# Kernel optimization log

Measured on AMD Instinct MI355X. Metric: run time of the kernel, lower is better.

## Reference

```python
import jax, jax.numpy as jnp
import numpy as np

EPS = 1.1920929e-7  # torch.finfo(float32).eps, default for F.rms_norm
ATTN_SCALE = 0.1
ROPE_BASE = 10000.0


def _rms_norm(x):
    # F.rms_norm over last dim, no learned weight
    return x * jax.lax.rsqrt(jnp.mean(x * x, axis=-1, keepdims=True) + EPS)


def _rotary(x):
    # x: [B, T, H, D]; rotates halves as in the Rotary module
    T, D = x.shape[1], x.shape[3]
    half = D // 2
    inv_freq = 1.0 / (ROPE_BASE ** (jnp.arange(0, D, 2, dtype=jnp.float32) / D))  # [half]
    freqs = jnp.arange(T, dtype=jnp.float32)[:, None] * inv_freq[None, :]          # [T, half]
    cos = jnp.cos(freqs)[None, :, None, :]
    sin = jnp.sin(freqs)[None, :, None, :]
    x1, x2 = x[..., :half], x[..., half:]
    return jnp.concatenate([x1 * cos + x2 * sin, -x1 * sin + x2 * cos], axis=-1)


def setup_inputs() -> dict:
    key = jax.random.key(0)
    ks = jax.random.split(key, 8)
    B, T, dim, H, hd = 2, 2048, 1024, 16, 64
    gate_in = 12
    s = 1.0 / np.sqrt(dim)
    return {
        "x": jax.random.normal(ks[0], (B, T, dim), dtype=jnp.float32),
        "v1": jax.random.normal(ks[1], (B, T, H, hd), dtype=jnp.float32),
        "Wq": jax.random.uniform(ks[2], (dim, dim), jnp.float32, -s, s),
        "Wk": jax.random.uniform(ks[3], (dim, dim), jnp.float32, -s, s),
        "Wv": jax.random.uniform(ks[4], (dim, dim), jnp.float32, -s, s),
        "Wproj": jax.random.uniform(ks[5], (dim, dim), jnp.float32, -s, s),
        "Wg": jax.random.uniform(ks[6], (H, gate_in), jnp.float32,
                                  -1.0 / np.sqrt(gate_in), 1.0 / np.sqrt(gate_in)),
        "lamb": jnp.float32(0.5),
    }


def reference(x, v1, Wq, Wk, Wv, Wproj, Wg, lamb):
    B, T, dim = x.shape
    H, hd = v1.shape[2], v1.shape[3]
    q = (x @ Wq.T).reshape(B, T, H, hd)
    k = (x @ Wk.T).reshape(B, T, H, hd)
    v = (x @ Wv.T).reshape(B, T, H, hd)
    # value-residual mixing
    v = (1.0 - lamb) * v + lamb * v1
    # QK RMSNorm + RoPE
    q = _rotary(_rms_norm(q))
    k = _rotary(_rms_norm(k))
    # causal SDPA with fixed scale
    scores = jnp.einsum('bqhd,bkhd->bhqk', q, k) * ATTN_SCALE
    causal = jnp.tril(jnp.ones((T, T), dtype=bool))
    scores = jnp.where(causal[None, None], scores, jnp.float32(-jnp.inf))
    probs = jax.nn.softmax(scores, axis=-1)
    y = jnp.einsum('bhqk,bkhd->bqhd', probs, v)  # [B, T, H, hd]
    # sigmoid gate from first 12 channels of x
    gate = jax.nn.sigmoid(x[..., :Wg.shape[1]] @ Wg.T)  # [B, T, H]
    y = y * gate[..., None]
    y = y.reshape(B, T, H * hd) @ Wproj.T
    return y
```

## Files before the change

kernel.cpp:

```cpp
#include <hip/hip_runtime.h>
#include <math.h>


#define B_    2
#define T_    2048
#define DIM_  1024
#define H_    16
#define HD_   64
#define NROW  (B_ * T_)
#define EPS_  1.1920929e-07f
#define SCALE_ 0.1f
#define LOG2_10K 13.287712379549449f
#define INV2PI 0.15915494309189535f

typedef unsigned short u16;
typedef unsigned int   u32;
typedef __bf16 bf16x8 __attribute__((ext_vector_type(8)));
typedef __bf16 bf16x2 __attribute__((ext_vector_type(2)));
typedef float  f32x4  __attribute__((ext_vector_type(4)));

__device__ __forceinline__ u16 f2b(float f) {
  u32 u = __float_as_uint(f);
  u += 0x7fffu + ((u >> 16) & 1u);
  return (u16)(u >> 16);
}
__device__ __forceinline__ u32 pk2(float a, float b) {
#if __has_builtin(__builtin_amdgcn_cvt_pk_bf16_f32)
  bf16x2 r = __builtin_amdgcn_cvt_pk_bf16_f32(a, b);
  return __builtin_bit_cast(u32, r);
#else
  return (u32)f2b(a) | ((u32)f2b(b) << 16);
#endif
}
__device__ __forceinline__ void fast_sincos_rev(float rev, float* s, float* c) {
  const float r = rev - floorf(rev);
#if __has_builtin(__builtin_amdgcn_sinf) && __has_builtin(__builtin_amdgcn_cosf)
  *s = __builtin_amdgcn_sinf(r);
  *c = __builtin_amdgcn_cosf(r);
#else
  *s = __sinf(r * 6.283185307179586f);
  *c = __cosf(r * 6.283185307179586f);
#endif
}
#define MFMA16(a,b,c) __builtin_amdgcn_mfma_f32_16x16x32_bf16((a),(b),(c),0,0,0)

__global__ __launch_bounds__(256) void convert_all(
    const float* __restrict__ x, const float* __restrict__ Wq,
    const float* __restrict__ Wk, const float* __restrict__ Wv,
    const float* __restrict__ Wp,
    u16* __restrict__ xb, u16* __restrict__ wb ) {
  const int i = blockIdx.x * 256 + threadIdx.x;
  const float* src;
  u16* dst;
  int off;
  if (i < 1048576)       { src = x;  dst = xb;            off = i; }
  else if (i < 1310720)  { src = Wq; dst = wb;            off = i - 1048576; }
  else if (i < 1572864)  { src = Wk; dst = wb + 1048576;  off = i - 1310720; }
  else if (i < 1835008)  { src = Wv; dst = wb + 2097152;  off = i - 1572864; }
  else                   { src = Wp; dst = wb + 3145728;  off = i - 1835008; }
  const float4 f = ((const float4*)src)[off];
  uint2 o;
  o.x = pk2(f.x, f.y);
  o.y = pk2(f.z, f.w);
  ((uint2*)dst)[off] = o;
}

template <bool IS_PROJ>
__global__ __launch_bounds__(256) void gemm_rp(
    const u16* __restrict__ Ab, const u16* __restrict__ Wb,
    u16* __restrict__ qo, u16* __restrict__ ko, u16* __restrict__ vto,
    float* __restrict__ fo, const float* __restrict__ v1,
    const float* __restrict__ lambp) {
  __shared__ __attribute__((aligned(16))) unsigned char Asm[8192];
  __shared__ __attribute__((aligned(16))) unsigned char Bsm[8192];
  const int tid  = threadIdx.x;
  const int w    = tid >> 6;
  const int lane = tid & 63;
  const int lo = lane & 15, hi = lane >> 4;
  const int m0 = blockIdx.x << 7;
  const int by = blockIdx.y;
  const int mode = IS_PROJ ? 3 : (by >> 3);
  const int n0 = IS_PROJ ? (by << 7) : ((by & 7) << 7);
  const u16* W = IS_PROJ ? Wb : (Wb + (size_t)mode * (DIM_ * DIM_));

  const int wm = w & 1, wn = w >> 1;

  const u16* agA0 = Ab + (size_t)(m0 + (2 * w + 0) * 16 + lo) * DIM_ + (hi << 3);
  const u16* agA1 = Ab + (size_t)(m0 + (2 * w + 1) * 16 + lo) * DIM_ + (hi << 3);
  const u16* agB0 = W  + (size_t)(n0 + (2 * w + 0) * 16 + lo) * DIM_ + (hi << 3);
  const u16* agB1 = W  + (size_t)(n0 + (2 * w + 1) * 16 + lo) * DIM_ + (hi << 3);
  unsigned char* dA0 = Asm + (2 * w + 0) * 1024 + (lane << 4);
  unsigned char* dA1 = Asm + (2 * w + 1) * 1024 + (lane << 4);
  unsigned char* dB0 = Bsm + (2 * w + 0) * 1024 + (lane << 4);
  unsigned char* dB1 = Bsm + (2 * w + 1) * 1024 + (lane << 4);

  f32x4 acc[4][4];
#pragma unroll
  for (int i = 0; i < 4; ++i)
#pragma unroll
    for (int j = 0; j < 4; ++j) acc[i][j] = (f32x4){0.f, 0.f, 0.f, 0.f};

  uint4 ra0 = *(const uint4*)agA0;
  uint4 ra1 = *(const uint4*)agA1;
  uint4 rb0 = *(const uint4*)agB0;
  uint4 rb1 = *(const uint4*)agB1;
  agA0 += 32; agA1 += 32; agB0 += 32; agB1 += 32;

  for (int kc = 0; kc < DIM_; kc += 32) {
    __syncthreads();
    *(uint4*)dA0 = ra0;
    *(uint4*)dA1 = ra1;
    *(uint4*)dB0 = rb0;
    *(uint4*)dB1 = rb1;
    __syncthreads();
    if (kc + 32 < DIM_) {
      ra0 = *(const uint4*)agA0;
      ra1 = *(const uint4*)agA1;
      rb0 = *(const uint4*)agB0;
      rb1 = *(const uint4*)agB1;
      agA0 += 32; agA1 += 32; agB0 += 32; agB1 += 32;
    }
    bf16x8 bfr[4];
#pragma unroll
    for (int nt = 0; nt < 4; ++nt)
      bfr[nt] = *(const bf16x8*)(Bsm + (((wn * 4 + nt) * 64 + lane) << 4));
#pragma unroll
    for (int mt = 0; mt < 4; ++mt) {
      const bf16x8 af = *(const bf16x8*)(Asm + (((wm * 4 + mt) * 64 + lane) << 4));
#pragma unroll
      for (int nt = 0; nt < 4; ++nt)
        acc[mt][nt] = MFMA16(af, bfr[nt], acc[mt][nt]);
    }
  }

  const int head = (n0 >> 6) + wn;
  if (mode <= 1) {
    u16* C = (mode == 0) ? qo : ko;
    const float if0 = exp2f(-(float)lo * (LOG2_10K / 32.f)) * INV2PI;
    const float if1 = exp2f(-(float)(lo + 16) * (LOG2_10K / 32.f)) * INV2PI;
#pragma unroll
    for (int mt = 0; mt < 4; ++mt)
#pragma unroll
      for (int r = 0; r < 4; ++r) {
        float ss = 0.f;
#pragma unroll
        for (int nt = 0; nt < 4; ++nt) { const float v = acc[mt][nt][r]; ss += v * v; }
        ss += __shfl_xor(ss, 1, 64); ss += __shfl_xor(ss, 2, 64);
        ss += __shfl_xor(ss, 4, 64); ss += __shfl_xor(ss, 8, 64);
        const float scl = rsqrtf(ss * (1.f / 64.f) + EPS_);
        const int row_g = m0 + wm * 64 + mt * 16 + hi * 4 + r;
        const float tpos = (float)(row_g & (T_ - 1));
        float sn0, cs0, sn1, cs1;
        fast_sincos_rev(tpos * if0, &sn0, &cs0);
        fast_sincos_rev(tpos * if1, &sn1, &cs1);
        u16* crow = C + (size_t)row_g * DIM_ + head * HD_;
        const float x10 = acc[mt][0][r] * scl, x11 = acc[mt][1][r] * scl;
        const float x20 = acc[mt][2][r] * scl, x21 = acc[mt][3][r] * scl;
        crow[lo]      = f2b(x10 * cs0 + x20 * sn0);
        crow[16 + lo] = f2b(x11 * cs1 + x21 * sn1);
        crow[32 + lo] = f2b(x20 * cs0 - x10 * sn0);
        crow[48 + lo] = f2b(x21 * cs1 - x11 * sn1);
      }
  } else if (mode == 2) {
    const float lam = lambp[0];
#pragma unroll
    for (int mt = 0; mt < 4; ++mt)
#pragma unroll
      for (int r = 0; r < 4; ++r) {
        const int row_g = m0 + wm * 64 + mt * 16 + hi * 4 + r;
        const int bb = row_g >> 11, tt = row_g & (T_ - 1);
        const int bh = bb * H_ + head;
        const float* v1r = v1 + (size_t)row_g * DIM_ + head * HD_;
#pragma unroll
        for (int nt = 0; nt < 4; ++nt) {
          const int d = nt * 16 + lo;
          const float ov = (1.f - lam) * acc[mt][nt][r] + lam * v1r[d];
          vto[((size_t)(bh * HD_ + d)) * T_ + tt] = f2b(ov);
        }
      }
  } else {
#pragma unroll
    for (int mt = 0; mt < 4; ++mt)
#pragma unroll
      for (int r = 0; r < 4; ++r) {
        const int row_g = m0 + wm * 64 + mt * 16 + hi * 4 + r;
        float* orow = fo + (size_t)row_g * DIM_ + n0 + wn * 64;
#pragma unroll
        for (int nt = 0; nt < 4; ++nt) orow[nt * 16 + lo] = acc[mt][nt][r];
      }
  }
}

__global__ __launch_bounds__(256) void gate_kernel(
    const float* __restrict__ x, const float* __restrict__ Wg,
    float* __restrict__ gate) {
  const int id = blockIdx.x * 256 + threadIdx.x;
  const int n = id >> 4, h = id & 15;
  const float* xr = x + (size_t)n * DIM_;
  const float* wr = Wg + h * 12;
  float s = 0.f;
#pragma unroll
  for (int j = 0; j < 12; ++j) s += xr[j] * wr[j];
  gate[id] = 1.f / (1.f + __expf(-s));
}

__global__ __launch_bounds__(256) void attn3(
    const u16* __restrict__ q, const u16* __restrict__ k, const u16* __restrict__ vt,
    const float* __restrict__ gate, u16* __restrict__ y) {
  __shared__ __attribute__((aligned(16))) unsigned char smem[16384];
  const int tid = threadIdx.x;
  const int wv = tid >> 6, lane = tid & 63, lo = lane & 15, hi = lane >> 4;
  const int idx = blockIdx.x;
  const int qt = 31 - (idx >> 5);
  const int bh = idx & 31;
  const int b = bh >> 4, h = bh & 15;
  const int qb = qt << 6;

  const int qrow = b * T_ + qb + wv * 16 + lo;
  const u16* qp = q + (size_t)qrow * DIM_ + h * HD_;
  const bf16x8 qf0 = *(const bf16x8*)(qp + hi * 8);
  const bf16x8 qf1 = *(const bf16x8*)(qp + 32 + hi * 8);

  f32x4 o[4];
#pragma unroll
  for (int i = 0; i < 4; ++i) o[i] = (f32x4){0.f, 0.f, 0.f, 0.f};
  float mrun = -1e30f, lrun = 0.f;

  const int sl = tid & 63, skh = (tid >> 6) & 1, st0 = tid >> 7;
  const int srow = sl & 15, skk = skh * 32 + ((sl >> 4) << 3);
  const u16* kg0 = k + ((size_t)(b * T_ + st0 * 16 + srow)) * DIM_ + h * HD_ + skk;
  const u16* kg1 = kg0 + (size_t)32 * DIM_;
  const u16* vg0 = vt + ((size_t)(bh * HD_ + st0 * 16 + srow)) * T_ + skk;
  const u16* vg1 = vg0 + (size_t)32 * T_;

  uint4 kr0 = *(const uint4*)kg0, kr1 = *(const uint4*)kg1;
  uint4 vr0 = *(const uint4*)vg0, vr1 = *(const uint4*)vg1;

  const int off0 = tid << 4, off1 = (tid + 256) << 4;

  for (int tix = 0; tix <= qt; ++tix) {
    __syncthreads();
    *(uint4*)(smem + off0) = kr0;
    *(uint4*)(smem + off1) = kr1;
    *(uint4*)(smem + 8192 + off0) = vr0;
    *(uint4*)(smem + 8192 + off1) = vr1;
    if (tix < qt) {
      const size_t ko = (size_t)(tix + 1) * 64 * DIM_;
      const size_t vo = (size_t)(tix + 1) * 64;
      kr0 = *(const uint4*)(kg0 + ko); kr1 = *(const uint4*)(kg1 + ko);
      vr0 = *(const uint4*)(vg0 + vo); vr1 = *(const uint4*)(vg1 + vo);
    }
    __syncthreads();

    f32x4 stl[4];
#pragma unroll
    for (int kt = 0; kt < 4; ++kt) stl[kt] = (f32x4){0.f, 0.f, 0.f, 0.f};
#pragma unroll
    for (int kh = 0; kh < 2; ++kh) {
      const bf16x8 qb_ = kh ? qf1 : qf0;
#pragma unroll
      for (int kt = 0; kt < 4; ++kt) {
        const bf16x8 af = *(const bf16x8*)(smem + (((kt * 2 + kh) * 64 + lane) << 4));
        stl[kt] = MFMA16(af, qb_, stl[kt]);
      }
    }
    const bool diag = (tix == qt);
#pragma unroll
    for (int kt = 0; kt < 4; ++kt)
#pragma unroll
      for (int r = 0; r < 4; ++r) {
        float s = stl[kt][r] * SCALE_;
        if (diag && (kt * 16 + hi * 4 + r > wv * 16 + lo)) s = -3e38f;
        stl[kt][r] = s;
      }
    float mx = stl[0][0];
#pragma unroll
    for (int kt = 0; kt < 4; ++kt)
#pragma unroll
      for (int r = 0; r < 4; ++r) mx = fmaxf(mx, stl[kt][r]);
    mx = fmaxf(mx, __shfl_xor(mx, 16, 64));
    mx = fmaxf(mx, __shfl_xor(mx, 32, 64));
    const float mn = fmaxf(mrun, mx);
    const float alpha = __expf(mrun - mn);
    mrun = mn;
    float ps = 0.f;
#pragma unroll
    for (int kt = 0; kt < 4; ++kt)
#pragma unroll
      for (int r = 0; r < 4; ++r) { stl[kt][r] = __expf(stl[kt][r] - mn); ps += stl[kt][r]; }
    ps += __shfl_xor(ps, 16, 64);
    ps += __shfl_xor(ps, 32, 64);
    lrun = lrun * alpha + ps;
#pragma unroll
    for (int dt = 0; dt < 4; ++dt) o[dt] *= alpha;

    u32 pkv[4][2];
#pragma unroll
    for (int kt = 0; kt < 4; ++kt) {
      pkv[kt][0] = pk2(stl[kt][0], stl[kt][1]);
      pkv[kt][1] = pk2(stl[kt][2], stl[kt][3]);
    }
#pragma unroll
    for (int kh = 0; kh < 2; ++kh) {
      uint4 w4;
      u32* w4p = (u32*)&w4;
#pragma unroll
      for (int wd = 0; wd < 4; ++wd) {
        const int src = (2 * (hi & 1) + (wd >> 1)) * 16 + lo;
        const u32 a  = (u32)__shfl((int)pkv[2 * kh][wd & 1], src, 64);
        const u32 bb = (u32)__shfl((int)pkv[2 * kh + 1][wd & 1], src, 64);
        w4p[wd] = (hi < 2) ? a : bb;
      }
      const bf16x8 pf = __builtin_bit_cast(bf16x8, w4);
#pragma unroll
      for (int dt = 0; dt < 4; ++dt) {
        const bf16x8 vf = *(const bf16x8*)(smem + 8192 + (((dt * 2 + kh) * 64 + lane) << 4));
        o[dt] = MFMA16(vf, pf, o[dt]);
      }
    }
  }

  const float inv = gate[(size_t)qrow * H_ + h] / lrun;
  u16* yrow = y + (size_t)qrow * DIM_ + h * HD_;
#pragma unroll
  for (int dt = 0; dt < 4; ++dt) {
    ushort4 pq;
    pq.x = f2b(o[dt][0] * inv); pq.y = f2b(o[dt][1] * inv);
    pq.z = f2b(o[dt][2] * inv); pq.w = f2b(o[dt][3] * inv);
    *(ushort4*)(yrow + dt * 16 + hi * 4) = pq;
  }
}

extern "C" void kernel_launch(void* const* d_in, const int* in_sizes, int n_in,
                              void* d_out, int out_size, void* d_ws, size_t ws_size,
                              hipStream_t stream) {
  const float* x    = (const float*)d_in[0];
  const float* v1   = (const float*)d_in[1];
  const float* Wq   = (const float*)d_in[2];
  const float* Wk   = (const float*)d_in[3];
  const float* Wv   = (const float*)d_in[4];
  const float* Wp   = (const float*)d_in[5];
  const float* Wg   = (const float*)d_in[6];
  const float* lamb = (const float*)d_in[7];

  const size_t NX = (size_t)NROW * DIM_;
  const size_t NW = (size_t)DIM_ * DIM_;

  u16* q  = (u16*)d_ws;
  u16* k  = q + NX;
  u16* vt = k + NX;
  u16* xb = vt + NX;
  u16* wb = xb + NX;
  float* gate = (float*)(wb + 4 * NW);

  const dim3 bb(256);

  convert_all<<<dim3(8192), bb, 0, stream>>>(x, Wq, Wk, Wv, Wp, xb, wb);
  gemm_rp<false><<<dim3(NROW / 128, 24), bb, 0, stream>>>(
      xb, wb, q, k, vt, nullptr, v1, lamb);
  gate_kernel<<<dim3(NROW * H_ / 256), bb, 0, stream>>>(x, Wg, gate);
  attn3<<<dim3(B_ * H_ * (T_ / 64)), bb, 0, stream>>>(q, k, vt, gate, q);
  gemm_rp<true><<<dim3(NROW / 128, 8), bb, 0, stream>>>(
      q, wb + 3 * NW, nullptr, nullptr, nullptr, (float*)d_out, nullptr, nullptr);
}
```

Before: 238.7 us.

## Double-buffer GEMM tiles in LDS using direct global-to-LDS loads

Replaces the register-staged global loads and LDS stores in the GEMM main loop with global_load_lds instructions that write straight into shared memory. Shared memory is split into two buffers so the next k-chunk is fetched while the current one feeds the MFMAs, leaving one barrier per iteration instead of two. This removes VGPR staging and the extra LDS store instructions, but doubles LDS use per block, which may reduce occupancy. It also relies on the barrier alone to make the asynchronous LDS writes visible, with no explicit vmcnt wait.

```diff
diff --git a/kernel.cpp b/kernel.cpp
--- a/kernel.cpp
+++ b/kernel.cpp
@@ -43,6 +43,12 @@
 #endif
 }
 #define MFMA16(a,b,c) __builtin_amdgcn_mfma_f32_16x16x32_bf16((a),(b),(c),0,0,0)
+
+typedef const __attribute__((address_space(1))) unsigned char gbuf_t;
+typedef __attribute__((address_space(3))) unsigned char lbuf_t;
+__device__ __forceinline__ void gload_lds16(const u16* g, unsigned char* l) {
+  __builtin_amdgcn_global_load_lds((gbuf_t*)g, (lbuf_t*)l, 16, 0, 0);
+}
 
 __global__ __launch_bounds__(256) void convert_all(
     const float* __restrict__ x, const float* __restrict__ Wq,
@@ -71,8 +77,7 @@
     u16* __restrict__ qo, u16* __restrict__ ko, u16* __restrict__ vto,
     float* __restrict__ fo, const float* __restrict__ v1,
     const float* __restrict__ lambp) {
-  __shared__ __attribute__((aligned(16))) unsigned char Asm[8192];
-  __shared__ __attribute__((aligned(16))) unsigned char Bsm[8192];
+  __shared__ __attribute__((aligned(16))) unsigned char sm[32768];
   const int tid  = threadIdx.x;
   const int w    = tid >> 6;
   const int lane = tid & 63;
@@ -89,10 +94,6 @@
   const u16* agA1 = Ab + (size_t)(m0 + (2 * w + 1) * 16 + lo) * DIM_ + (hi << 3);
   const u16* agB0 = W  + (size_t)(n0 + (2 * w + 0) * 16 + lo) * DIM_ + (hi << 3);
   const u16* agB1 = W  + (size_t)(n0 + (2 * w + 1) * 16 + lo) * DIM_ + (hi << 3);
-  unsigned char* dA0 = Asm + (2 * w + 0) * 1024 + (lane << 4);
-  unsigned char* dA1 = Asm + (2 * w + 1) * 1024 + (lane << 4);
-  unsigned char* dB0 = Bsm + (2 * w + 0) * 1024 + (lane << 4);
-  unsigned char* dB1 = Bsm + (2 * w + 1) * 1024 + (lane << 4);
 
   f32x4 acc[4][4];
 #pragma unroll
@@ -100,37 +101,43 @@
 #pragma unroll
     for (int j = 0; j < 4; ++j) acc[i][j] = (f32x4){0.f, 0.f, 0.f, 0.f};
 
-  uint4 ra0 = *(const uint4*)agA0;
-  uint4 ra1 = *(const uint4*)agA1;
-  uint4 rb0 = *(const uint4*)agB0;
-  uint4 rb1 = *(const uint4*)agB1;
-  agA0 += 32; agA1 += 32; agB0 += 32; agB1 += 32;
-
+  {
+    unsigned char* ad = sm + (2 * w) * 1024;
+    unsigned char* bd = sm + 8192 + (2 * w) * 1024;
+    gload_lds16(agA0, ad);
+    gload_lds16(agA1, ad + 1024);
+    gload_lds16(agB0, bd);
+    gload_lds16(agB1, bd + 1024);
+    agA0 += 32; agA1 += 32; agB0 += 32; agB1 += 32;
+  }
+  __syncthreads();
+
+  int buf = 0;
   for (int kc = 0; kc < DIM_; kc += 32) {
-    __syncthreads();
-    *(uint4*)dA0 = ra0;
-    *(uint4*)dA1 = ra1;
-    *(uint4*)dB0 = rb0;
-    *(uint4*)dB1 = rb1;
-    __syncthreads();
     if (kc + 32 < DIM_) {
-      ra0 = *(const uint4*)agA0;
-      ra1 = *(const uint4*)agA1;
-      rb0 = *(const uint4*)agB0;
-      rb1 = *(const uint4*)agB1;
+      unsigned char* ad = sm + ((buf ^ 1) << 14) + (2 * w) * 1024;
+      unsigned char* bd = ad + 8192;
+      gload_lds16(agA0, ad);
+      gload_lds16(agA1, ad + 1024);
+      gload_lds16(agB0, bd);
+      gload_lds16(agB1, bd + 1024);
       agA0 += 32; agA1 += 32; agB0 += 32; agB1 += 32;
     }
+    const unsigned char* Acur = sm + (buf << 14);
+    const unsigned char* Bcur = Acur + 8192;
     bf16x8 bfr[4];
 #pragma unroll
     for (int nt = 0; nt < 4; ++nt)
-      bfr[nt] = *(const bf16x8*)(Bsm + (((wn * 4 + nt) * 64 + lane) << 4));
+      bfr[nt] = *(const bf16x8*)(Bcur + (((wn * 4 + nt) * 64 + lane) << 4));
 #pragma unroll
     for (int mt = 0; mt < 4; ++mt) {
-      const bf16x8 af = *(const bf16x8*)(Asm + (((wm * 4 + mt) * 64 + lane) << 4));
+      const bf16x8 af = *(const bf16x8*)(Acur + (((wm * 4 + mt) * 64 + lane) << 4));
 #pragma unroll
       for (int nt = 0; nt < 4; ++nt)
         acc[mt][nt] = MFMA16(af, bfr[nt], acc[mt][nt]);
     }
+    if (kc + 32 < DIM_) __syncthreads();
+    buf ^= 1;
   }
 
   const int head = (n0 >> 6) + wn;
```

Result: no change. 235.3 us (-1.4%).
